# Performance work log

Measured on AMD Instinct MI355X. Metric: run time of the kernel, lower is better.

Reference implementation:

```python
import jax, jax.numpy as jnp
import numpy as np

N, E, D, ED, L = 40000, 640000, 128, 16, 3  # nodes, edges, emb_dim, edge_dim, num_layer
BN_EPS = 1e-5


def setup_inputs() -> dict:
    key = jax.random.key(0)
    ks = jax.random.split(key, 20)
    s = 0.05
    inp = {
        "x": jax.random.normal(ks[0], (N, D), jnp.float32),
        "edge_attr": jax.random.normal(ks[1], (E, ED), jnp.float32),
        # node encoder Linear(input_dim, emb_dim)
        "node_W": jax.random.normal(ks[2], (D, D), jnp.float32) * s,
        "node_b": jnp.zeros((D,), jnp.float32),
        # per-layer params (leading dim L)
        "edge_W": jax.random.normal(ks[3], (L, ED, D), jnp.float32) * s,
        "edge_b": jnp.zeros((L, D), jnp.float32),
        "attn_W": jax.random.normal(ks[4], (L, 2 * D, 1), jnp.float32) * s,
        "attn_b": jnp.zeros((L, 1), jnp.float32),
        "eps": jnp.zeros((L,), jnp.float32),
        "W1": jax.random.normal(ks[5], (L, D, 2 * D), jnp.float32) * s,
        "b1": jnp.zeros((L, 2 * D), jnp.float32),
        "bn1_g": jnp.ones((L, 2 * D), jnp.float32),
        "bn1_b": jnp.zeros((L, 2 * D), jnp.float32),
        "W2": jax.random.normal(ks[6], (L, 2 * D, D), jnp.float32) * s,
        "b2": jnp.zeros((L, D), jnp.float32),
        "bn_g": jnp.ones((L, D), jnp.float32),
        "bn_b": jnp.zeros((L, D), jnp.float32),
        "edge_index": jax.random.randint(ks[7], (2, E), 0, N, jnp.int32),
    }
    return inp


def _bn_eval(h, g, b):
    # BatchNorm1d in eval with running_mean=0, running_var=1
    return g * h * (1.0 / np.sqrt(1.0 + BN_EPS)) + b


def reference(x, edge_attr, node_W, node_b, edge_W, edge_b, attn_W, attn_b,
              eps, W1, b1, bn1_g, bn1_b, W2, b2, bn_g, bn_b, edge_index):
    src, dst = edge_index[0], edge_index[1]
    h = x @ node_W + node_b  # node_encoder, [N, D]
    for l in range(L):
        e = edge_attr @ edge_W[l] + edge_b[l]       # [E, D] edge embedding
        xj = h[src]                                  # [E, D] source gather
        xi = h[dst]                                  # [E, D] target gather
        a = jax.nn.sigmoid(jnp.concatenate([xi, xj], axis=-1) @ attn_W[l] + attn_b[l])  # [E,1]
        msg = jax.nn.relu(xj * a + e)                # fused per-edge message
        agg = jax.ops.segment_sum(msg, dst, num_segments=N)  # scatter-add aggregate
        z = (1.0 + eps[l]) * h + agg
        # GIN mlp: Linear -> BN(eval) -> ReLU -> Linear
        z = _bn_eval(z @ W1[l] + b1[l], bn1_g[l], bn1_b[l])
        z = jax.nn.relu(z)
        z = z @ W2[l] + b2[l]
        # outer BatchNorm(eval); dropout = identity in eval; JK='last', no residual
        z = _bn_eval(z, bn_g[l], bn_b[l])
        if l < L - 1:
            z = jax.nn.relu(z)
        h = z
    return h
```

## Files before the change

kernel.cpp:

```cpp
#include <hip/hip_runtime.h>
#include <math.h>

#define NN 40000
#define EE 640000
#define DD 128
#define EDD 16
#define LL 3
#define TEB 64

__device__ __constant__ float kBnInv = 0.9999950000374997f;

typedef __bf16 bf16x8 __attribute__((ext_vector_type(8)));
typedef float  f32x4  __attribute__((ext_vector_type(4)));
typedef float  f32x2  __attribute__((ext_vector_type(2)));

__device__ __forceinline__ unsigned pack_bf2(float a, float b) {
    unsigned ua = __float_as_uint(a), ub = __float_as_uint(b);
    ua = (ua + 0x7fffu + ((ua >> 16) & 1u)) >> 16;
    ub = (ub + 0x7fffu + ((ub >> 16) & 1u)) & 0xffff0000u;
    return ua | ub;
}
__device__ __forceinline__ unsigned short bf16r(float x) {
    unsigned u = __float_as_uint(x);
    u = (u + 0x7fffu + ((u >> 16) & 1u)) >> 16;
    return (unsigned short)u;
}

__global__ __launch_bounds__(256) void node_enc_kernel(
    const float* __restrict__ x, const float* __restrict__ W,
    const float* __restrict__ b,
    const float* __restrict__ aW, const float* __restrict__ eps_p,
    float* __restrict__ h, unsigned* __restrict__ hb,
    float* __restrict__ pi, float* __restrict__ pj, float* __restrict__ z)
{
    __shared__ float xs[32][DD];
    const int t = threadIdx.x;
    const long rowbase = (long)blockIdx.x * 32;

    const float4* x4 = (const float4*)(x + rowbase * DD);
    float4* xs4 = (float4*)&xs[0][0];
#pragma unroll
    for (int i = 0; i < 4; i++) xs4[t + i * 256] = x4[t + i * 256];
    __syncthreads();

    const int c  = (t & 31) * 4;
    const int r0 = (t >> 5) * 4;

    float acc[4][4] = {};
    for (int k4 = 0; k4 < DD; k4 += 4) {
        float4 xr[4];
#pragma unroll
        for (int i = 0; i < 4; i++) xr[i] = *(const float4*)&xs[r0 + i][k4];
#pragma unroll
        for (int kk = 0; kk < 4; kk++) {
            const float4 w = *(const float4*)(W + (k4 + kk) * DD + c);
#pragma unroll
            for (int i = 0; i < 4; i++) {
                const float xv = ((const float*)&xr[i])[kk];
                acc[i][0] = fmaf(xv, w.x, acc[i][0]);
                acc[i][1] = fmaf(xv, w.y, acc[i][1]);
                acc[i][2] = fmaf(xv, w.z, acc[i][2]);
                acc[i][3] = fmaf(xv, w.w, acc[i][3]);
            }
        }
    }
    const float4 bv  = *(const float4*)(b + c);
    const float4 awi = *(const float4*)(aW + c);
    const float4 awj = *(const float4*)(aW + DD + c);
    const float ep = 1.0f + eps_p[0];

    float pa[4], pb[4];
#pragma unroll
    for (int i = 0; i < 4; i++) {
        const long row = rowbase + r0 + i;
        float4 ov = { acc[i][0] + bv.x, acc[i][1] + bv.y,
                      acc[i][2] + bv.z, acc[i][3] + bv.w };
        *(float4*)(h + row * DD + c) = ov;
        uint2 pv = { pack_bf2(ov.x, ov.y), pack_bf2(ov.z, ov.w) };
        *(uint2*)(hb + row * 64 + (c >> 1)) = pv;
        float4 zv = { ep * ov.x, ep * ov.y, ep * ov.z, ep * ov.w };
        *(float4*)(z + row * DD + c) = zv;
        pa[i] = ov.x * awi.x + ov.y * awi.y + ov.z * awi.z + ov.w * awi.w;
        pb[i] = ov.x * awj.x + ov.y * awj.y + ov.z * awj.z + ov.w * awj.w;
    }
#pragma unroll
    for (int off = 1; off < 32; off <<= 1) {
#pragma unroll
        for (int i = 0; i < 4; i++) {
            pa[i] += __shfl_xor(pa[i], off, 64);
            pb[i] += __shfl_xor(pb[i], off, 64);
        }
    }
    if ((t & 31) == 0) {
#pragma unroll
        for (int i = 0; i < 4; i++) {
            pi[rowbase + r0 + i] = pa[i];
            pj[rowbase + r0 + i] = pb[i];
        }
    }
}

__global__ __launch_bounds__(256) void wcast_kernel(
    const float* __restrict__ W1, const float* __restrict__ W2,
    unsigned short* __restrict__ w1t, unsigned short* __restrict__ w2t)
{
    const int idx = blockIdx.x * 256 + threadIdx.x;
    const int l = idx >> 15, r = idx & 32767;
    {   const int n = r >> 7, k = r & 127;
        w1t[idx] = bf16r(W1[(l << 15) + (k << 8) + n]);
    }
    {   const int n = r >> 8, k = r & 255;
        w2t[idx] = bf16r(W2[(l << 15) + (k << 7) + n]);
    }
}

__global__ __launch_bounds__(256) void hist_kernel(
    const int* __restrict__ edge_index, int* __restrict__ counts)
{
    const int i = blockIdx.x * 256 + threadIdx.x;
    atomicAdd(&counts[edge_index[EE + i]], 1);
}

__global__ __launch_bounds__(256) void scan1_kernel(
    const int* __restrict__ counts, int* __restrict__ scanned,
    int* __restrict__ partials)
{
    __shared__ int sdata[256];
    const int t = threadIdx.x;
    const int base = blockIdx.x * 1024 + t * 4;
    int v[4]; int sum = 0;
#pragma unroll
    for (int i = 0; i < 4; i++) {
        const int idx = base + i;
        v[i] = (idx < NN) ? counts[idx] : 0;
        sum += v[i];
    }
    sdata[t] = sum;
    __syncthreads();
    for (int off = 1; off < 256; off <<= 1) {
        int x = (t >= off) ? sdata[t - off] : 0;
        __syncthreads();
        sdata[t] += x;
        __syncthreads();
    }
    int run = sdata[t] - sum;
#pragma unroll
    for (int i = 0; i < 4; i++) {
        const int idx = base + i;
        if (idx < NN) scanned[idx] = run;
        run += v[i];
    }
    if (t == 255) partials[blockIdx.x] = sdata[255];
}

__global__ void scan2_kernel(int* __restrict__ partials)
{
    if (threadIdx.x == 0) {
        int run = 0;
        for (int i = 0; i < 40; i++) { int v = partials[i]; partials[i] = run; run += v; }
    }
}

__global__ __launch_bounds__(256) void scan3_kernel(
    const int* __restrict__ scanned, const int* __restrict__ partials,
    int* __restrict__ offsets, int* __restrict__ cursor)
{
    const int idx = blockIdx.x * 256 + threadIdx.x;
    if (idx < NN) {
        const int off = scanned[idx] + partials[idx >> 10];
        offsets[idx] = off;
        cursor[idx]  = off;
    }
}

__global__ __launch_bounds__(256) void scatter_kernel(
    const int* __restrict__ edge_index, const float* __restrict__ edge_attr,
    int* __restrict__ cursor,
    int* __restrict__ srcs_p, int* __restrict__ dstd_p,
    unsigned* __restrict__ ea_b)
{
    const int i = blockIdx.x * 256 + threadIdx.x;
    const int src = edge_index[i];
    const int dst = edge_index[EE + i];
    const int pos = atomicAdd(&cursor[dst], 1);
    srcs_p[pos] = src << 6;
    dstd_p[pos] = dst << 7;

    const float4* sp = (const float4*)(edge_attr + (long)i * EDD);
    const float4 s0 = sp[0], s1 = sp[1], s2 = sp[2], s3 = sp[3];
    uint4 o0 = { pack_bf2(s0.x, s0.y), pack_bf2(s0.z, s0.w),
                 pack_bf2(s1.x, s1.y), pack_bf2(s1.z, s1.w) };
    uint4 o1 = { pack_bf2(s2.x, s2.y), pack_bf2(s2.z, s2.w),
                 pack_bf2(s3.x, s3.y), pack_bf2(s3.z, s3.w) };
    *(uint4*)(ea_b + (long)pos * 8)     = o0;
    *(uint4*)(ea_b + (long)pos * 8 + 4) = o1;
}

__global__ __launch_bounds__(256) void edge_msg_kernel(
    const unsigned* __restrict__ hb, const unsigned* __restrict__ ea_b,
    const float* __restrict__ pi, const float* __restrict__ pj,
    const int* __restrict__ srcs_p, const int* __restrict__ dstd_p,
    const float* __restrict__ ab_p,
    const float* __restrict__ eW, const float* __restrict__ eb,
    float* __restrict__ z)
{
    __shared__ unsigned sh_hb[TEB * 64];
    __shared__ float    sh_ea[TEB * EDD];
    __shared__ int      sh_src[TEB];
    __shared__ int      sh_dst[TEB];
    __shared__ float    sh_a[TEB];

    const int t = threadIdx.x;
    const long e0 = (long)blockIdx.x * TEB;

    if (t < TEB) {
        const int ss = srcs_p[e0 + t];
        const int dd = dstd_p[e0 + t];
        sh_src[t] = ss;
        sh_dst[t] = dd;
        const float s = pi[dd >> 7] + pj[ss >> 6] + ab_p[0];
        sh_a[t] = 1.0f / (1.0f + expf(-s));
    }
    __syncthreads();

    {
        const int chunk = t & 15;
        const int r0    = t >> 4;
#pragma unroll
        for (int i = 0; i < TEB / 16; i++) {
            const int row  = r0 + 16 * i;
            const int srow = sh_src[row];
            *(uint4*)&sh_hb[row * 64 + chunk * 4] =
                *(const uint4*)(hb + srow + chunk * 4);
        }
#pragma unroll
        for (int i = 0; i < 2; i++) {
            const int idx  = t * 2 + i;
            const int edge = idx >> 3, q = idx & 7;
            const unsigned u = ea_b[e0 * 8 + idx];
            float2 f = { __uint_as_float(u << 16),
                         __uint_as_float(u & 0xffff0000u) };
            *(float2*)&sh_ea[edge * EDD + q * 2] = f;
        }
    }
    __syncthreads();

    const int wid = t >> 6, lane = t & 63;
    const int c0 = lane * 2;
    const int base = wid * (TEB / 4);

    f32x2 ew[EDD];
#pragma unroll
    for (int q = 0; q < EDD; q++) {
        const float2 w2 = ((const float2*)(eW + q * DD))[lane];
        ew[q][0] = w2.x; ew[q][1] = w2.y;
    }
    const float2 ebf = ((const float2*)eb)[lane];
    const f32x2 ebv = { ebf.x, ebf.y };
    const f32x2 zero2 = { 0.0f, 0.0f };

    f32x2 acc = zero2;
    int cur = sh_dst[base];

#pragma unroll 4
    for (int j = 0; j < TEB / 4; j++) {
        const int   dd = sh_dst[base + j];
        const float a  = sh_a[base + j];
        const unsigned u = sh_hb[(base + j) * 64 + lane];

        const float4* eap = (const float4*)&sh_ea[(base + j) * EDD];
        const float4 t0 = eap[0], t1 = eap[1], t2 = eap[2], t3 = eap[3];
        const float ea[EDD] = { t0.x,t0.y,t0.z,t0.w, t1.x,t1.y,t1.z,t1.w,
                                t2.x,t2.y,t2.z,t2.w, t3.x,t3.y,t3.z,t3.w };
        f32x2 ev = ebv;
#pragma unroll
        for (int q = 0; q < EDD; q++) {
            const f32x2 eaq = { ea[q], ea[q] };
            ev = __builtin_elementwise_fma(eaq, ew[q], ev);
        }

        if (dd != cur) {
            atomicAdd(&z[cur + c0],     acc[0]);
            atomicAdd(&z[cur + c0 + 1], acc[1]);
            acc = zero2; cur = dd;
        }
        const f32x2 xj = { __uint_as_float(u << 16),
                           __uint_as_float(u & 0xffff0000u) };
        const f32x2 av = { a, a };
        f32x2 m = __builtin_elementwise_fma(xj, av, ev);
        m = __builtin_elementwise_max(m, zero2);
        acc += m;
    }
    atomicAdd(&z[cur + c0],     acc[0]);
    atomicAdd(&z[cur + c0 + 1], acc[1]);
}

__global__ __launch_bounds__(256) void mlp_mfma_kernel(
    const float* __restrict__ zin,
    const unsigned short* __restrict__ w1t, const unsigned short* __restrict__ w2t,
    const float* __restrict__ b1, const float* __restrict__ g1, const float* __restrict__ bb1,
    const float* __restrict__ b2, const float* __restrict__ g2, const float* __restrict__ bb2,
    const float* __restrict__ aWn, const float* __restrict__ epsn_p,
    float* __restrict__ out, unsigned* __restrict__ hb,
    float* __restrict__ pi, float* __restrict__ pj, float* __restrict__ z,
    const int do_relu)
{
    __shared__ __align__(16) unsigned short zsb[64][136];
    __shared__ __align__(16) unsigned short usb[64][264];
    __shared__ float sh_pi[64], sh_pj[64];
    const int t = threadIdx.x;
    const int wid = t >> 6, lane = t & 63;
    const long rowbase = (long)blockIdx.x * 64;

    if (t < 64) { sh_pi[t] = 0.0f; sh_pj[t] = 0.0f; }

    {
        const float4* z4 = (const float4*)(zin + rowbase * DD);
#pragma unroll
        for (int i = 0; i < 8; i++) {
            const int idx = t + i * 256;
            const float4 v = z4[idx];
            const int row = idx >> 5;
            const int c4  = (idx & 31) * 4;
            uint2 pv = { pack_bf2(v.x, v.y), pack_bf2(v.z, v.w) };
            *(uint2*)&zsb[row][c4] = pv;
        }
    }
    __syncthreads();

    const int mrow  = lane & 15;
    const int quad  = lane >> 4;
    const f32x4 vzero = {0.0f, 0.0f, 0.0f, 0.0f};

    {
        const int nt0 = wid * 4;
        bf16x8 bf[4][4];
#pragma unroll
        for (int j = 0; j < 4; j++) {
            const unsigned short* wp = w1t + ((nt0 + j) * 16 + mrow) * 128 + quad * 8;
#pragma unroll
            for (int ks = 0; ks < 4; ks++)
                bf[j][ks] = *(const bf16x8*)(wp + ks * 32);
        }
        float gg[4], bi[4], bt[4];
#pragma unroll
        for (int j = 0; j < 4; j++) {
            const int c = (nt0 + j) * 16 + mrow;
            gg[j] = g1[c]; bi[j] = b1[c]; bt[j] = bb1[c];
        }
#pragma unroll
        for (int rt = 0; rt < 4; rt++) {
            bf16x8 af[4];
#pragma unroll
            for (int ks = 0; ks < 4; ks++)
                af[ks] = *(const bf16x8*)&zsb[rt * 16 + mrow][ks * 32 + quad * 8];
            f32x4 acc[4];
#pragma unroll
            for (int j = 0; j < 4; j++) acc[j] = vzero;
#pragma unroll
            for (int j = 0; j < 4; j++)
#pragma unroll
                for (int ks = 0; ks < 4; ks++)
                    acc[j] = __builtin_amdgcn_mfma_f32_16x16x32_bf16(af[ks], bf[j][ks], acc[j], 0, 0, 0);
#pragma unroll
            for (int j = 0; j < 4; j++) {
                const int c = (nt0 + j) * 16 + mrow;
#pragma unroll
                for (int r = 0; r < 4; r++) {
                    const int row = rt * 16 + quad * 4 + r;
                    const float u = fmaxf(fmaf(gg[j] * (acc[j][r] + bi[j]), kBnInv, bt[j]), 0.0f);
                    const float up = __shfl_xor(u, 1, 64);
                    if ((mrow & 1) == 0)
                        *(unsigned*)&usb[row][c] = pack_bf2(u, up);
                }
            }
        }
    }
    __syncthreads();

    {
        const int nt0 = wid * 2;
        bf16x8 bf[2][8];
#pragma unroll
        for (int j = 0; j < 2; j++) {
            const unsigned short* wp = w2t + ((nt0 + j) * 16 + mrow) * 256 + quad * 8;
#pragma unroll
            for (int ks = 0; ks < 8; ks++)
                bf[j][ks] = *(const bf16x8*)(wp + ks * 32);
        }
        float gg[2], bi[2], bt[2], awi[2], awj[2];
#pragma unroll
        for (int j = 0; j < 2; j++) {
            const int c = (nt0 + j) * 16 + mrow;
            gg[j] = g2[c]; bi[j] = b2[c]; bt[j] = bb2[c];
            awi[j] = aWn[c]; awj[j] = aWn[DD + c];
        }
        const float epn = do_relu ? (1.0f + epsn_p[0]) : 0.0f;

#pragma unroll
        for (int rt = 0; rt < 4; rt++) {
            bf16x8 af[8];
#pragma unroll
            for (int ks = 0; ks < 8; ks++)
                af[ks] = *(const bf16x8*)&usb[rt * 16 + mrow][ks * 32 + quad * 8];
            f32x4 acc[2];
            acc[0] = vzero; acc[1] = vzero;
#pragma unroll
            for (int j = 0; j < 2; j++)
#pragma unroll
                for (int ks = 0; ks < 8; ks++)
                    acc[j] = __builtin_amdgcn_mfma_f32_16x16x32_bf16(af[ks], bf[j][ks], acc[j], 0, 0, 0);

            float si[4] = {0, 0, 0, 0}, sj[4] = {0, 0, 0, 0};
#pragma unroll
            for (int j = 0; j < 2; j++) {
                const int c = (nt0 + j) * 16 + mrow;
#pragma unroll
                for (int r = 0; r < 4; r++) {
                    const long row = rowbase + rt * 16 + quad * 4 + r;
                    float v = fmaf(gg[j] * (acc[j][r] + bi[j]), kBnInv, bt[j]);
                    if (do_relu) {
                        v = fmaxf(v, 0.0f);
                        z[row * DD + c] = epn * v;
                        si[r] = fmaf(v, awi[j], si[r]);
                        sj[r] = fmaf(v, awj[j], sj[r]);
                    }
                    out[row * DD + c] = v;
                    const float vp = __shfl_xor(v, 1, 64);
                    if ((mrow & 1) == 0)
                        hb[row * 64 + (c >> 1)] = pack_bf2(v, vp);
                }
            }
            if (do_relu) {
#pragma unroll
                for (int off = 1; off < 16; off <<= 1) {
#pragma unroll
                    for (int r = 0; r < 4; r++) {
                        si[r] += __shfl_xor(si[r], off, 64);
                        sj[r] += __shfl_xor(sj[r], off, 64);
                    }
                }
                if (mrow == 0) {
#pragma unroll
                    for (int r = 0; r < 4; r++) {
                        atomicAdd(&sh_pi[rt * 16 + quad * 4 + r], si[r]);
                        atomicAdd(&sh_pj[rt * 16 + quad * 4 + r], sj[r]);
                    }
                }
            }
        }
    }
    if (do_relu) {
        __syncthreads();
        if (t < 64) {
            pi[rowbase + t] = sh_pi[t];
            pj[rowbase + t] = sh_pj[t];
        }
    }
}

extern "C" void kernel_launch(void* const* d_in, const int* in_sizes, int n_in,
                              void* d_out, int out_size, void* d_ws, size_t ws_size,
                              hipStream_t stream)
{
    const float* x         = (const float*)d_in[0];
    const float* edge_attr = (const float*)d_in[1];
    const float* node_W    = (const float*)d_in[2];
    const float* node_b    = (const float*)d_in[3];
    const float* edge_W    = (const float*)d_in[4];
    const float* edge_b    = (const float*)d_in[5];
    const float* attn_W    = (const float*)d_in[6];
    const float* attn_b    = (const float*)d_in[7];
    const float* eps       = (const float*)d_in[8];
    const float* W1        = (const float*)d_in[9];
    const float* b1        = (const float*)d_in[10];
    const float* bn1_g     = (const float*)d_in[11];
    const float* bn1_b     = (const float*)d_in[12];
    const float* W2        = (const float*)d_in[13];
    const float* b2        = (const float*)d_in[14];
    const float* bn_g      = (const float*)d_in[15];
    const float* bn_b      = (const float*)d_in[16];
    const int*   edge_index= (const int*)d_in[17];

    float* h    = (float*)d_ws;
    float* z    = h + (size_t)NN * DD;
    float* pi   = z + (size_t)NN * DD;
    float* pj   = pi + NN;
    unsigned* ea_b = (unsigned*)(pj + NN);
    unsigned* hbuf = ea_b + (size_t)EE * 8;
    unsigned short* w1t = (unsigned short*)(hbuf + (size_t)NN * 64);
    unsigned short* w2t = w1t + (size_t)LL * 32768;
    int* counts  = (int*)(w2t + (size_t)LL * 32768);
    int* offsets = counts + NN;
    int* cursor  = offsets + NN;
    int* scanned = cursor + NN;
    int* partials= scanned + 40960;
    int* srcs_p  = partials + 64;
    int* dstd_p  = srcs_p + EE;
    float* out = (float*)d_out;

    node_enc_kernel<<<NN / 32, 256, 0, stream>>>(
        x, node_W, node_b, attn_W, eps, h, hbuf, pi, pj, z);
    wcast_kernel<<<LL * 128, 256, 0, stream>>>(W1, W2, w1t, w2t);

    hipMemsetAsync(counts, 0, NN * sizeof(int), stream);
    hist_kernel<<<EE / 256, 256, 0, stream>>>(edge_index, counts);
    scan1_kernel<<<40, 256, 0, stream>>>(counts, scanned, partials);
    scan2_kernel<<<1, 64, 0, stream>>>(partials);
    scan3_kernel<<<(NN + 255) / 256, 256, 0, stream>>>(scanned, partials, offsets, cursor);
    scatter_kernel<<<EE / 256, 256, 0, stream>>>(
        edge_index, edge_attr, cursor, srcs_p, dstd_p, ea_b);

    for (int l = 0; l < LL; l++) {
        const int ln = (l + 1 < LL) ? (l + 1) : l;
        edge_msg_kernel<<<EE / TEB, 256, 0, stream>>>(
            hbuf, ea_b, pi, pj, srcs_p, dstd_p, attn_b + l,
            edge_W + (size_t)l * EDD * DD, edge_b + (size_t)l * DD, z);
        mlp_mfma_kernel<<<NN / 64, 256, 0, stream>>>(
            z,
            w1t + (size_t)l * 32768, w2t + (size_t)l * 32768,
            b1 + (size_t)l * 2 * DD, bn1_g + (size_t)l * 2 * DD, bn1_b + (size_t)l * 2 * DD,
            b2 + (size_t)l * DD, bn_g + (size_t)l * DD, bn_b + (size_t)l * DD,
            attn_W + (size_t)ln * 2 * DD, eps + ln,
            (l == LL - 1) ? out : h, hbuf, pi, pj, z, (l < LL - 1) ? 1 : 0);
    }
}
```

Measured before the change: 523.8 us.

## Compute edge embeddings with bf16 MFMA and gather source rows into registers

The per-edge 16x128 edge-embedding projection, previously done with scalar FMAs per lane, now runs as a 32x32x16 bf16 MFMA per wave. It uses a pre-transposed bf16 copy of edge_W produced in the weight-cast kernel, and the result is staged in shared memory. Source node rows are gathered directly into registers instead of through shared memory. This cuts per-edge VALU work in the dominant edge kernel, at the cost of rounding edge_W to bf16 and a larger shared-memory footprint (32 KB per block) that could lower occupancy.

```diff
diff --git a/kernel.cpp b/kernel.cpp
--- a/kernel.cpp
+++ b/kernel.cpp
@@ -11,6 +11,7 @@
 __device__ __constant__ float kBnInv = 0.9999950000374997f;
 
 typedef __bf16 bf16x8 __attribute__((ext_vector_type(8)));
+typedef float  f32x16 __attribute__((ext_vector_type(16)));
 typedef float  f32x4  __attribute__((ext_vector_type(4)));
 typedef float  f32x2  __attribute__((ext_vector_type(2)));
 
@@ -102,7 +103,9 @@
 
 __global__ __launch_bounds__(256) void wcast_kernel(
     const float* __restrict__ W1, const float* __restrict__ W2,
-    unsigned short* __restrict__ w1t, unsigned short* __restrict__ w2t)
+    const float* __restrict__ eW,
+    unsigned short* __restrict__ w1t, unsigned short* __restrict__ w2t,
+    unsigned short* __restrict__ ewt)
 {
     const int idx = blockIdx.x * 256 + threadIdx.x;
     const int l = idx >> 15, r = idx & 32767;
@@ -111,6 +114,11 @@
     }
     {   const int n = r >> 8, k = r & 255;
         w2t[idx] = bf16r(W2[(l << 15) + (k << 7) + n]);
+    }
+    if (idx < LL * 2048) {
+        const int le = idx >> 11, re = idx & 2047;
+        const int n = re >> 4, k = re & 15;
+        ewt[idx] = bf16r(eW[(le << 11) + (k << 7) + n]);
     }
 }
 
@@ -201,16 +209,16 @@
     const float* __restrict__ pi, const float* __restrict__ pj,
     const int* __restrict__ srcs_p, const int* __restrict__ dstd_p,
     const float* __restrict__ ab_p,
-    const float* __restrict__ eW, const float* __restrict__ eb,
+    const unsigned short* __restrict__ eWt, const float* __restrict__ eb,
     float* __restrict__ z)
 {
-    __shared__ unsigned sh_hb[TEB * 64];
-    __shared__ float    sh_ea[TEB * EDD];
-    __shared__ int      sh_src[TEB];
-    __shared__ int      sh_dst[TEB];
-    __shared__ float    sh_a[TEB];
+    __shared__ float sh_e[TEB * DD];
+    __shared__ int   sh_src[TEB];
+    __shared__ int   sh_dst[TEB];
+    __shared__ float sh_a[TEB];
 
     const int t = threadIdx.x;
+    const int wid = t >> 6, lane = t & 63;
     const long e0 = (long)blockIdx.x * TEB;
 
     if (t < TEB) {
@@ -221,71 +229,56 @@
         const float s = pi[dd >> 7] + pj[ss >> 6] + ab_p[0];
         sh_a[t] = 1.0f / (1.0f + expf(-s));
     }
+
+    const int l31 = lane & 31, half = lane >> 5;
+    const int mt = wid & 1, nt0 = wid >> 1;
+    const bf16x8 afr  = *(const bf16x8*)(ea_b + (e0 + mt * 32 + l31) * 8 + half * 4);
+    const bf16x8 bfr0 = *(const bf16x8*)(eWt + (nt0 * 32 + l31) * 16 + half * 8);
+    const bf16x8 bfr1 = *(const bf16x8*)(eWt + ((nt0 + 2) * 32 + l31) * 16 + half * 8);
+
     __syncthreads();
 
+    const int base = wid * 16;
+    unsigned u[16];
+#pragma unroll
+    for (int j = 0; j < 16; j++)
+        u[j] = hb[sh_src[base + j] + lane];
+
     {
-        const int chunk = t & 15;
-        const int r0    = t >> 4;
-#pragma unroll
-        for (int i = 0; i < TEB / 16; i++) {
-            const int row  = r0 + 16 * i;
-            const int srow = sh_src[row];
-            *(uint4*)&sh_hb[row * 64 + chunk * 4] =
-                *(const uint4*)(hb + srow + chunk * 4);
-        }
-#pragma unroll
-        for (int i = 0; i < 2; i++) {
-            const int idx  = t * 2 + i;
-            const int edge = idx >> 3, q = idx & 7;
-            const unsigned u = ea_b[e0 * 8 + idx];
-            float2 f = { __uint_as_float(u << 16),
-                         __uint_as_float(u & 0xffff0000u) };
-            *(float2*)&sh_ea[edge * EDD + q * 2] = f;
+        f32x16 a0 = {0.0f,0.0f,0.0f,0.0f, 0.0f,0.0f,0.0f,0.0f,
+                     0.0f,0.0f,0.0f,0.0f, 0.0f,0.0f,0.0f,0.0f};
+        f32x16 a1 = a0;
+        a0 = __builtin_amdgcn_mfma_f32_32x32x16_bf16(afr, bfr0, a0, 0, 0, 0);
+        a1 = __builtin_amdgcn_mfma_f32_32x32x16_bf16(afr, bfr1, a1, 0, 0, 0);
+        const float eb0 = eb[nt0 * 32 + l31];
+        const float eb1 = eb[(nt0 + 2) * 32 + l31];
+        const int rb = mt * 32 + 4 * half;
+#pragma unroll
+        for (int r = 0; r < 16; r++) {
+            const int row = rb + (r & 3) + 8 * (r >> 2);
+            sh_e[row * DD + nt0 * 32 + l31]       = a0[r] + eb0;
+            sh_e[row * DD + (nt0 + 2) * 32 + l31] = a1[r] + eb1;
         }
     }
     __syncthreads();
 
-    const int wid = t >> 6, lane = t & 63;
     const int c0 = lane * 2;
-    const int base = wid * (TEB / 4);
-
-    f32x2 ew[EDD];
-#pragma unroll
-    for (int q = 0; q < EDD; q++) {
-        const float2 w2 = ((const float2*)(eW + q * DD))[lane];
-        ew[q][0] = w2.x; ew[q][1] = w2.y;
-    }
-    const float2 ebf = ((const float2*)eb)[lane];
-    const f32x2 ebv = { ebf.x, ebf.y };
     const f32x2 zero2 = { 0.0f, 0.0f };
-
     f32x2 acc = zero2;
     int cur = sh_dst[base];
 
-#pragma unroll 4
-    for (int j = 0; j < TEB / 4; j++) {
-        const int   dd = sh_dst[base + j];
-        const float a  = sh_a[base + j];
-        const unsigned u = sh_hb[(base + j) * 64 + lane];
-
-        const float4* eap = (const float4*)&sh_ea[(base + j) * EDD];
-        const float4 t0 = eap[0], t1 = eap[1], t2 = eap[2], t3 = eap[3];
-        const float ea[EDD] = { t0.x,t0.y,t0.z,t0.w, t1.x,t1.y,t1.z,t1.w,
-                                t2.x,t2.y,t2.z,t2.w, t3.x,t3.y,t3.z,t3.w };
-        f32x2 ev = ebv;
-#pragma unroll
-        for (int q = 0; q < EDD; q++) {
-            const f32x2 eaq = { ea[q], ea[q] };
-            ev = __builtin_elementwise_fma(eaq, ew[q], ev);
-        }
-
+#pragma unroll
+    for (int j = 0; j < 16; j++) {
+        const int dd = sh_dst[base + j];
         if (dd != cur) {
             atomicAdd(&z[cur + c0],     acc[0]);
             atomicAdd(&z[cur + c0 + 1], acc[1]);
             acc = zero2; cur = dd;
         }
-        const f32x2 xj = { __uint_as_float(u << 16),
-                           __uint_as_float(u & 0xffff0000u) };
+        const float a = sh_a[base + j];
+        const f32x2 ev = *(const f32x2*)&sh_e[(base + j) * DD + c0];
+        const f32x2 xj = { __uint_as_float(u[j] << 16),
+                           __uint_as_float(u[j] & 0xffff0000u) };
         const f32x2 av = { a, a };
         f32x2 m = __builtin_elementwise_fma(xj, av, ev);
         m = __builtin_elementwise_max(m, zero2);
@@ -490,7 +483,8 @@
     unsigned* hbuf = ea_b + (size_t)EE * 8;
     unsigned short* w1t = (unsigned short*)(hbuf + (size_t)NN * 64);
     unsigned short* w2t = w1t + (size_t)LL * 32768;
-    int* counts  = (int*)(w2t + (size_t)LL * 32768);
+    unsigned short* ewt = w2t + (size_t)LL * 32768;
+    int* counts  = (int*)(ewt + (size_t)LL * 2048);
     int* offsets = counts + NN;
     int* cursor  = offsets + NN;
     int* scanned = cursor + NN;
@@ -501,7 +495,7 @@
 
     node_enc_kernel<<<NN / 32, 256, 0, stream>>>(
         x, node_W, node_b, attn_W, eps, h, hbuf, pi, pj, z);
-    wcast_kernel<<<LL * 128, 256, 0, stream>>>(W1, W2, w1t, w2t);
+    wcast_kernel<<<LL * 128, 256, 0, stream>>>(W1, W2, edge_W, w1t, w2t, ewt);
 
     hipMemsetAsync(counts, 0, NN * sizeof(int), stream);
     hist_kernel<<<EE / 256, 256, 0, stream>>>(edge_index, counts);
@@ -515,7 +509,7 @@
         const int ln = (l + 1 < LL) ? (l + 1) : l;
         edge_msg_kernel<<<EE / TEB, 256, 0, stream>>>(
             hbuf, ea_b, pi, pj, srcs_p, dstd_p, attn_b + l,
-            edge_W + (size_t)l * EDD * DD, edge_b + (size_t)l * DD, z);
+            ewt + (size_t)l * 2048, edge_b + (size_t)l * DD, z);
         mlp_mfma_kernel<<<NN / 64, 256, 0, stream>>>(
             z,
             w1t + (size_t)l * 32768, w2t + (size_t)l * 32768,
```

Result: no change. 533.1 us (+1.8%).
